# Optimization experiments

Hardware: AMD Instinct MI355X
Metric: run time of the kernel (lower is better)

## Reference

```python
import jax, jax.numpy as jnp
import numpy as np
from jax import lax

DIM = 192
HEADS = 6
WIDTH = 256
HEIGHT = 128
BATCH = 2


def _conv1x1(x, w):
    # x: [b,c,h,w], w: [o,c] (1x1 conv, no bias)
    return jnp.einsum('bchw,oc->bohw', x, w)


def setup_inputs() -> dict:
    key = jax.random.key(0)
    ks = jax.random.split(key, 7)
    c = DIM
    std = c ** -0.5
    x = jax.random.normal(ks[0], (BATCH, c, HEIGHT, WIDTH), dtype=jnp.float32)
    rpb_table = 0.02 * jax.random.normal(ks[1], (2 * WIDTH - 1, HEADS), dtype=jnp.float32)
    w_qkv = std * jax.random.normal(ks[2], (3 * c, c), dtype=jnp.float32)
    w_depth = (1.0 / 3.0) * jax.random.normal(ks[3], (3 * c, 1, 3, 3), dtype=jnp.float32)
    w_pre = std * jax.random.normal(ks[4], (c, c), dtype=jnp.float32)
    w_out = std * jax.random.normal(ks[5], (c, c), dtype=jnp.float32)
    w_gate = std * jax.random.normal(ks[6], (c, c), dtype=jnp.float32)
    return {"x": x, "rpb_table": rpb_table, "w_qkv": w_qkv, "w_depth": w_depth,
            "w_pre": w_pre, "w_out": w_out, "w_gate": w_gate, "num_heads": HEADS}


def reference(x, rpb_table, w_qkv, w_depth, w_pre, w_out, w_gate, num_heads):
    b, c, h, w = x.shape
    hd = c // num_heads
    scale = hd ** -0.5

    x_gate = jax.nn.silu(_conv1x1(x, w_gate))

    t = _conv1x1(x, w_qkv)  # [b, 3c, h, w]
    qkv = lax.conv_general_dilated(
        t, w_depth, window_strides=(1, 1), padding='SAME',
        feature_group_count=3 * c,
        dimension_numbers=('NCHW', 'OIHW', 'NCHW'))
    q, k, v = jnp.split(qkv, 3, axis=1)

    def _rows(z):
        # 'b (head c) h w -> b h head w c'
        return z.reshape(b, num_heads, hd, h, w).transpose(0, 3, 1, 4, 2)

    q = _rows(q) * scale
    k = _rows(k)
    v = _rows(v)

    attn = jnp.einsum('bhnic,bhnjc->bhnij', q, k)  # [b, h, heads, w, w]

    # relative position bias: index[i, j] = i - j + (w - 1)
    idx = jnp.arange(w)[:, None] - jnp.arange(w)[None, :] + (w - 1)
    bias = rpb_table[idx].transpose(2, 0, 1)  # [heads, w, w]
    attn = jax.nn.softmax(attn + bias[None, None], axis=-1)

    out = jnp.einsum('bhnij,bhnjc->bhnic', attn, v)
    # 'b h head w c -> b (head c) h w'
    out = out.transpose(0, 2, 4, 1, 3).reshape(b, c, h, w)

    out = _conv1x1(out, w_pre) * x_gate
    return _conv1x1(out, w_out)
```

## Files before the change

### kernel.cpp

```cpp
#include <hip/hip_runtime.h>
#include <hip/hip_bf16.h>
#include <math.h>

#define BATCH 2
#define C 192
#define H 128
#define W 256
#define HEADS 6
#define HD 32
#define HW (H * W)
#define C3 (3 * C)
#define NPX (BATCH * HW)

typedef unsigned short ushort_t;
using bf16x8 = __attribute__((ext_vector_type(8))) short;
using f32x4  = __attribute__((ext_vector_type(4))) float;

static __device__ __forceinline__ float bfbits2f(ushort_t u) {
    return __uint_as_float(((unsigned)u) << 16);
}
static __device__ __forceinline__ ushort_t f2bfbits(float f) {
    __hip_bfloat16 h = __float2bfloat16(f);
    return *reinterpret_cast<ushort_t*>(&h);
}

__global__ __launch_bounds__(256) void prep_w_kernel(
    const float* __restrict__ wq, const float* __restrict__ wg,
    const float* __restrict__ wp, const float* __restrict__ wo,
    ushort_t* __restrict__ dst)
{
    const int i = blockIdx.x * 256 + threadIdx.x;
    const float* src; int off, base;
    if (i < 27648)      { src = wq; off = i;         base = 0; }
    else if (i < 36864) { src = wg; off = i - 27648; base = 110592; }
    else if (i < 46080) { src = wp; off = i - 36864; base = 147456; }
    else                { src = wo; off = i - 46080; base = 184320; }
    float4 v = ((const float4*)src)[off];
    if (i < 9216) {
        const float sc = 0.17677669529663687f;
        v.x *= sc; v.y *= sc; v.z *= sc; v.w *= sc;
    }
    ushort4 o;
    o.x = f2bfbits(v.x); o.y = f2bfbits(v.y);
    o.z = f2bfbits(v.z); o.w = f2bfbits(v.w);
    *(ushort4*)(dst + base + off * 4) = o;
}

__global__ __launch_bounds__(256) void transpose_x_kernel(
    const float* __restrict__ x, ushort_t* __restrict__ xt)
{
    __shared__ uint Xs[64 * 97];
    const int p0 = blockIdx.x * 64;
    const int b  = p0 >> 15, hw0 = p0 & (HW - 1);
    const int t  = threadIdx.x;

    {
        const int px = t & 63, g = t >> 6;
        const float* xb = x + (size_t)b * C * HW + hw0 + px;
#pragma unroll
        for (int i = 0; i < 24; ++i) {
            const int cp = g + i * 4;
            const float v0 = xb[(size_t)(2 * cp) * HW];
            const float v1 = xb[(size_t)(2 * cp + 1) * HW];
            Xs[px * 97 + cp] = (uint)f2bfbits(v0) | ((uint)f2bfbits(v1) << 16);
        }
    }
    __syncthreads();
    {
        const int px = t >> 2, grp = t & 3;
        uint* dst = (uint*)(xt + (size_t)(p0 + px) * C) + grp * 24;
        const uint* s = &Xs[px * 97 + grp * 24];
#pragma unroll
        for (int i = 0; i < 6; ++i) {
            uint4 u;
            u.x = s[i * 4 + 0]; u.y = s[i * 4 + 1];
            u.z = s[i * 4 + 2]; u.w = s[i * 4 + 3];
            *(uint4*)(dst + i * 4) = u;
        }
    }
}

template <int MODE, int OUTKIND, int MT>
__global__ __launch_bounds__(256) void conv_mfma_kernel(
    const ushort_t* __restrict__ in_t, const ushort_t* __restrict__ w_bf,
    void* __restrict__ outp, const ushort_t* __restrict__ gate, int ostride)
{
    const int lin = blockIdx.x;
    const int xcd = lin & 7;
    const int jj  = lin >> 3;
    const int pin = jj / MT;
    const int m   = jj - pin * MT;
    const int m0  = m * 64;
    const int p0  = (xcd * 16 + pin) * 512;

    const int t  = threadIdx.x;
    const int wv = t >> 6, lane = t & 63, quad = lane >> 4, l16 = lane & 15;

    __shared__ ushort_t As[64 * 200];
    {
        const int row = t >> 2, cg = (t & 3) * 48;
        const ushort_t* src = w_bf + (size_t)(m0 + row) * C + cg;
        ushort_t* dst = &As[row * 200 + cg];
#pragma unroll
        for (int i = 0; i < 6; ++i)
            *(bf16x8*)(dst + i * 8) = *(const bf16x8*)(src + i * 8);
    }
    __syncthreads();

    f32x4 acc[4][8];
#pragma unroll
    for (int rt = 0; rt < 4; ++rt)
#pragma unroll
        for (int ct = 0; ct < 8; ++ct) acc[rt][ct] = f32x4{0.f, 0.f, 0.f, 0.f};

    const ushort_t* bp = in_t + (size_t)(p0 + wv * 128 + l16) * C + quad * 8;

    bf16x8 bF[8], bFn[8];
#pragma unroll
    for (int ct = 0; ct < 8; ++ct)
        bF[ct] = *(const bf16x8*)(bp + (size_t)(ct * 16) * C);

#pragma unroll
    for (int ks = 0; ks < 6; ++ks) {
        if (ks < 5) {
#pragma unroll
            for (int ct = 0; ct < 8; ++ct)
                bFn[ct] = *(const bf16x8*)(bp + (size_t)(ct * 16) * C +
                                           (ks + 1) * 32);
        }
        bf16x8 aF[4];
#pragma unroll
        for (int rt = 0; rt < 4; ++rt)
            aF[rt] = *(const bf16x8*)&As[(rt * 16 + l16) * 200 + quad * 8 + ks * 32];
#pragma unroll
        for (int rt = 0; rt < 4; ++rt)
#pragma unroll
            for (int ct = 0; ct < 8; ++ct)
                acc[rt][ct] = __builtin_amdgcn_mfma_f32_16x16x32_bf16(
                    aF[rt], bF[ct], acc[rt][ct], 0, 0, 0);
#pragma unroll
        for (int ct = 0; ct < 8; ++ct) bF[ct] = bFn[ct];
    }

#pragma unroll
    for (int rt = 0; rt < 4; ++rt)
#pragma unroll
        for (int ct = 0; ct < 8; ++ct) {
            f32x4 v = acc[rt][ct];
            if (MODE == 1) {
#pragma unroll
                for (int r = 0; r < 4; ++r)
                    v[r] = v[r] / (1.f + __expf(-v[r]));
            }
            acc[rt][ct] = v;
        }

    if constexpr (OUTKIND == 0) {
        ushort_t* ob = (ushort_t*)outp;
#pragma unroll
        for (int rt = 0; rt < 4; ++rt)
#pragma unroll
            for (int ct = 0; ct < 8; ++ct) {
                const int px = p0 + wv * 128 + ct * 16 + l16;
                const int ch = m0 + rt * 16 + quad * 4;
                f32x4 v = acc[rt][ct];
                if (MODE == 2) {
                    const ushort4 g = *(const ushort4*)(gate + (size_t)px * C + ch);
                    v[0] *= bfbits2f(g.x); v[1] *= bfbits2f(g.y);
                    v[2] *= bfbits2f(g.z); v[3] *= bfbits2f(g.w);
                }
                ushort4 o;
                o.x = f2bfbits(v[0]); o.y = f2bfbits(v[1]);
                o.z = f2bfbits(v[2]); o.w = f2bfbits(v[3]);
                *(ushort4*)(ob + (size_t)px * ostride + ch) = o;
            }
    } else {
        const int bb = p0 >> 15;
        const int hwb = (p0 & (HW - 1)) + wv * 128;
        float* ob = (float*)outp + ((size_t)bb * C + m0) * HW + hwb;
#pragma unroll
        for (int rt = 0; rt < 4; ++rt)
#pragma unroll
            for (int ct = 0; ct < 8; ++ct) {
                const f32x4 v = acc[rt][ct];
#pragma unroll
                for (int r = 0; r < 4; ++r)
                    ob[(size_t)(rt * 16 + quad * 4 + r) * HW + ct * 16 + l16] = v[r];
            }
    }
}

__global__ __launch_bounds__(256) void dwconv3x3_px_kernel(
    const ushort_t* __restrict__ tin, const float* __restrict__ wd,
    ushort_t* __restrict__ out)
{
    __shared__ float wloc[576];
    const int cb  = blockIdx.y;
    const int tid = threadIdx.x;
    if (tid < 144)
        *(float4*)&wloc[tid * 4] = *(const float4*)(wd + cb * 576 + tid * 4);
    __syncthreads();

    const int chloc = (tid & 7) * 8;
    const int px = blockIdx.x * 128 + (tid >> 3) * 4;
    const int x0 = px & (W - 1);
    const int y  = (px >> 8) & (H - 1);

    const ushort_t* tb = tin + (size_t)px * C3 + cb * 64 + chloc;

    float acc[4][8];
#pragma unroll
    for (int i = 0; i < 4; ++i)
#pragma unroll
        for (int k = 0; k < 8; ++k) acc[i][k] = 0.f;

#pragma unroll
    for (int dy = -1; dy <= 1; ++dy) {
        const int yy = y + dy;
        if (yy < 0 || yy >= H) continue;
        const ushort_t* rp = tb + (ptrdiff_t)dy * W * C3;

        float f[6][8];
#pragma unroll
        for (int d = 0; d < 6; ++d) {
            const int xx = x0 + d - 1;
            if (xx < 0 || xx >= W) {
#pragma unroll
                for (int k = 0; k < 8; ++k) f[d][k] = 0.f;
            } else {
                const bf16x8 v = *(const bf16x8*)(rp + (ptrdiff_t)(d - 1) * C3);
#pragma unroll
                for (int k = 0; k < 8; ++k) f[d][k] = bfbits2f((ushort_t)v[k]);
            }
        }
#pragma unroll
        for (int k = 0; k < 8; ++k) {
            const float* wk = &wloc[(chloc + k) * 9 + (dy + 1) * 3];
            const float w0 = wk[0], w1 = wk[1], w2 = wk[2];
#pragma unroll
            for (int i = 0; i < 4; ++i)
                acc[i][k] += f[i][k] * w0 + f[i + 1][k] * w1 + f[i + 2][k] * w2;
        }
    }

    ushort_t* ob = out + (size_t)px * C3 + cb * 64 + chloc;
#pragma unroll
    for (int i = 0; i < 4; ++i) {
        bf16x8 o;
#pragma unroll
        for (int k = 0; k < 8; ++k) o[k] = (short)f2bfbits(acc[i][k]);
        *(bf16x8*)(ob + (size_t)i * C3) = o;
    }
}

__global__ __launch_bounds__(256) void attention_mfma_kernel(
    const ushort_t* __restrict__ qkv, const float* __restrict__ rpb,
    ushort_t* __restrict__ att)
{
    const int y    = blockIdx.x;
    const int head = blockIdx.y;
    const int b    = blockIdx.z;
    const int t    = threadIdx.x;
    const int wv   = t >> 6;
    const int lane = t & 63;
    const int quad = lane >> 4;
    const int l16  = lane & 15;

    __shared__ __align__(16) char smem[61952];
    ushort_t* Ks  = (ushort_t*)smem;
    ushort_t* Vt  = (ushort_t*)(smem + 20480);
    ushort_t* Qs  = (ushort_t*)(smem + 37376);
    ushort_t* rb4 = (ushort_t*)(smem + 57856);
    float*    Ol  = (float*)smem;

    const ushort_t* rowp = qkv + ((size_t)b * HW + (size_t)y * W + t) * C3 +
                           head * HD;
    bf16x8 vfr[4];
#pragma unroll
    for (int g = 0; g < 4; ++g) {
        *(bf16x8*)&Qs[t * 40 + g * 8] = *(const bf16x8*)(rowp + g * 8);
        *(bf16x8*)&Ks[t * 40 + g * 8] = *(const bf16x8*)(rowp + C + g * 8);
        vfr[g] = *(const bf16x8*)(rowp + 2 * C + g * 8);
    }
#pragma unroll
    for (int g = 0; g < 4; ++g)
#pragma unroll
        for (int k = 0; k < 8; ++k)
            Vt[(g * 8 + k) * 264 + t] = (ushort_t)vfr[g][k];

#pragma unroll
    for (int s = 0; s < 4; ++s) {
        const int k1 = t, k2 = 256 + t;
        const float v1 = (k1 + s < 511) ? rpb[(k1 + s) * HEADS + head] : 0.f;
        const float v2 = (k2 + s < 511) ? rpb[(k2 + s) * HEADS + head] : 0.f;
        rb4[s * 512 + k1] = f2bfbits(v1);
        rb4[s * 512 + k2] = f2bfbits(v2);
    }
    __syncthreads();

    bf16x8 aQ[4];
#pragma unroll
    for (int rt = 0; rt < 4; ++rt) {
        const int row = wv * 64 + rt * 16 + l16;
        aQ[rt] = *(const bf16x8*)&Qs[row * 40 + quad * 8];
    }
    __syncthreads();
    ushort_t* Pb = Qs + wv * 2560;

    float l_acc[16];
#pragma unroll
    for (int i = 0; i < 16; ++i) l_acc[i] = 0.f;
    f32x4 o_acc[4][2];
#pragma unroll
    for (int rt = 0; rt < 4; ++rt)
#pragma unroll
        for (int ct = 0; ct < 2; ++ct)
            o_acc[rt][ct] = f32x4{0.f, 0.f, 0.f, 0.f};

    for (int c2 = 0; c2 < 8; ++c2) {
#pragma unroll
        for (int half = 0; half < 2; ++half) {
            const int n = c2 * 2 + half;
            const bf16x8 bK = *(const bf16x8*)&Ks[(n * 16 + l16) * 40 + quad * 8];
#pragma unroll
            for (int rt = 0; rt < 4; ++rt) {
                const int base = wv * 64 + rt * 16 + quad * 4 - (n * 16 + l16) + 255;
                const int r0 = base & 3;
                const uint2 raw = *(const uint2*)(rb4 + r0 * 512 + (base - r0));
                f32x4 s;
                s[0] = __uint_as_float(raw.x << 16);
                s[1] = __uint_as_float(raw.x & 0xffff0000u);
                s[2] = __uint_as_float(raw.y << 16);
                s[3] = __uint_as_float(raw.y & 0xffff0000u);
                s = __builtin_amdgcn_mfma_f32_16x16x32_bf16(aQ[rt], bK, s, 0, 0, 0);
#pragma unroll
                for (int reg = 0; reg < 4; ++reg) {
                    const float p = __expf(s[reg]);
                    l_acc[rt * 4 + reg] += p;
                    Pb[(rt * 16 + quad * 4 + reg) * 40 + half * 16 + l16] =
                        f2bfbits(p);
                }
            }
        }
#pragma unroll
        for (int rt = 0; rt < 4; ++rt) {
            const bf16x8 aP = *(const bf16x8*)&Pb[(rt * 16 + l16) * 40 + quad * 8];
#pragma unroll
            for (int ct = 0; ct < 2; ++ct) {
                const bf16x8 bV = *(const bf16x8*)
                    &Vt[(ct * 16 + l16) * 264 + c2 * 32 + quad * 8];
                o_acc[rt][ct] = __builtin_amdgcn_mfma_f32_16x16x32_bf16(
                    aP, bV, o_acc[rt][ct], 0, 0, 0);
            }
        }
    }

#pragma unroll
    for (int i = 0; i < 16; ++i) {
        float v = l_acc[i];
        v += __shfl_xor(v, 1);
        v += __shfl_xor(v, 2);
        v += __shfl_xor(v, 4);
        v += __shfl_xor(v, 8);
        l_acc[i] = 1.f / v;
    }

    __syncthreads();
#pragma unroll
    for (int rt = 0; rt < 4; ++rt) {
        const int i = wv * 64 + rt * 16 + quad * 4;
#pragma unroll
        for (int ct = 0; ct < 2; ++ct) {
            const int c = ct * 16 + l16;
#pragma unroll
            for (int reg = 0; reg < 4; ++reg)
                Ol[c * 257 + i + reg] = o_acc[rt][ct][reg] * l_acc[rt * 4 + reg];
        }
    }
    __syncthreads();

    ushort_t* op = att + ((size_t)b * HW + (size_t)y * W + t) * C + head * HD;
#pragma unroll
    for (int g8 = 0; g8 < 4; ++g8) {
        bf16x8 o;
#pragma unroll
        for (int k = 0; k < 8; ++k)
            o[k] = (short)f2bfbits(Ol[(g8 * 8 + k) * 257 + t]);
        *(bf16x8*)(op + g8 * 8) = o;
    }
}

extern "C" void kernel_launch(void* const* d_in, const int* in_sizes, int n_in,
                              void* d_out, int out_size, void* d_ws, size_t ws_size,
                              hipStream_t stream)
{
    const float* x       = (const float*)d_in[0];
    const float* rpb     = (const float*)d_in[1];
    const float* w_qkv   = (const float*)d_in[2];
    const float* w_depth = (const float*)d_in[3];
    const float* w_pre   = (const float*)d_in[4];
    const float* w_out   = (const float*)d_in[5];
    const float* w_gate  = (const float*)d_in[6];
    float* out = (float*)d_out;

    char* wsb = (char*)d_ws;
    ushort_t* wbf      = (ushort_t*)wsb;
    ushort_t* w_qkv_b  = wbf;
    ushort_t* w_gate_b = wbf + 110592;
    ushort_t* w_pre_b  = wbf + 147456;
    ushort_t* w_out_b  = wbf + 184320;
    ushort_t* gate_t   = (ushort_t*)(wsb + 524288u);
    ushort_t* buf_t    = (ushort_t*)(wsb + 25690112u);
    ushort_t* att_t    = (ushort_t*)(wsb + 25690112u);
    ushort_t* y_t      = (ushort_t*)(wsb + 50855936u);
    ushort_t* buf_qkv  = (ushort_t*)(wsb + 101187584u);
    ushort_t* x_t      = (ushort_t*)(wsb + 101187584u);

    dim3 blk(256);

    prep_w_kernel<<<dim3(216), blk, 0, stream>>>(w_qkv, w_gate, w_pre, w_out, wbf);
    transpose_x_kernel<<<dim3(NPX / 64), blk, 0, stream>>>(x, x_t);
    conv_mfma_kernel<1, 0, 3><<<dim3(384), blk, 0, stream>>>(
        x_t, w_gate_b, gate_t, nullptr, C);
    conv_mfma_kernel<0, 0, 9><<<dim3(1152), blk, 0, stream>>>(
        x_t, w_qkv_b, buf_t, nullptr, C3);
    dwconv3x3_px_kernel<<<dim3(NPX / 128, 9), blk, 0, stream>>>(
        buf_t, w_depth, buf_qkv);
    attention_mfma_kernel<<<dim3(H, HEADS, BATCH), blk, 0, stream>>>(
        buf_qkv, rpb, att_t);
    conv_mfma_kernel<2, 0, 3><<<dim3(384), blk, 0, stream>>>(
        att_t, w_pre_b, y_t, gate_t, C);
    conv_mfma_kernel<0, 1, 3><<<dim3(384), blk, 0, stream>>>(
        y_t, w_out_b, out, nullptr, C);
}
```

Baseline: 351.2 us.

## Restructure attention: compute S transposed, exp2 softmax, direct-global Q/K loads, smaller LDS

The attention kernel now computes the transposed score tile (K as the A operand, Q as B), so each lane holds four consecutive key columns of one query row. P can then be written to LDS as a single packed 64-bit store, and the row sums reduce with two shuffles instead of four per row. Scale and bias are pre-multiplied by log2(e) so the kernel can use the hardware exp2 directly. Q and K fragments are read straight from global memory, with the next K fragment prefetched, which removes the Q/K staging in LDS and one barrier. LDS use drops from about 62 KB to about 39 KB and launch bounds request 4 blocks per CU for higher occupancy, at the cost of uncoalesced strided global reads for the K fragments.

```diff
diff --git a/kernel.cpp b/kernel.cpp
--- a/kernel.cpp
+++ b/kernel.cpp
@@ -37,7 +37,7 @@
     else                { src = wo; off = i - 46080; base = 184320; }
     float4 v = ((const float4*)src)[off];
     if (i < 9216) {
-        const float sc = 0.17677669529663687f;
+        const float sc = 0.25503488f;
         v.x *= sc; v.y *= sc; v.z *= sc; v.w *= sc;
     }
     ushort4 o;
@@ -253,7 +253,7 @@
     }
 }
 
-__global__ __launch_bounds__(256) void attention_mfma_kernel(
+__global__ __launch_bounds__(256, 4) void attention_mfma_kernel(
     const ushort_t* __restrict__ qkv, const float* __restrict__ rpb,
     ushort_t* __restrict__ att)
 {
@@ -266,50 +266,51 @@
     const int quad = lane >> 4;
     const int l16  = lane & 15;
 
-    __shared__ __align__(16) char smem[61952];
-    ushort_t* Ks  = (ushort_t*)smem;
-    ushort_t* Vt  = (ushort_t*)(smem + 20480);
-    ushort_t* Qs  = (ushort_t*)(smem + 37376);
-    ushort_t* rb4 = (ushort_t*)(smem + 57856);
-    float*    Ol  = (float*)smem;
-
-    const ushort_t* rowp = qkv + ((size_t)b * HW + (size_t)y * W + t) * C3 +
-                           head * HD;
-    bf16x8 vfr[4];
-#pragma unroll
-    for (int g = 0; g < 4; ++g) {
-        *(bf16x8*)&Qs[t * 40 + g * 8] = *(const bf16x8*)(rowp + g * 8);
-        *(bf16x8*)&Ks[t * 40 + g * 8] = *(const bf16x8*)(rowp + C + g * 8);
-        vfr[g] = *(const bf16x8*)(rowp + 2 * C + g * 8);
-    }
-#pragma unroll
-    for (int g = 0; g < 4; ++g)
-#pragma unroll
-        for (int k = 0; k < 8; ++k)
-            Vt[(g * 8 + k) * 264 + t] = (ushort_t)vfr[g][k];
-
-#pragma unroll
-    for (int s = 0; s < 4; ++s) {
-        const int k1 = t, k2 = 256 + t;
-        const float v1 = (k1 + s < 511) ? rpb[(k1 + s) * HEADS + head] : 0.f;
-        const float v2 = (k2 + s < 511) ? rpb[(k2 + s) * HEADS + head] : 0.f;
-        rb4[s * 512 + k1] = f2bfbits(v1);
-        rb4[s * 512 + k2] = f2bfbits(v2);
-    }
-    __syncthreads();
+    __shared__ __align__(16) char smem[39424];
+    ushort_t* Vt = (ushort_t*)smem;
+    ushort_t* Pb = (ushort_t*)(smem + 16896);
+    ushort_t* rb = (ushort_t*)(smem + 37376);
+    float*    Ol = (float*)smem;
+
+    const size_t rowbase = ((size_t)b * HW + (size_t)y * W) * C3;
+    const ushort_t* qbase = qkv + rowbase + head * HD + quad * 8;
+    const ushort_t* kbase = qbase + C;
+
+    {
+        const ushort_t* rowp = qkv + rowbase + (size_t)t * C3 + head * HD;
+        bf16x8 vfr[4];
+#pragma unroll
+        for (int g = 0; g < 4; ++g)
+            vfr[g] = *(const bf16x8*)(rowp + 2 * C + g * 8);
+#pragma unroll
+        for (int g = 0; g < 4; ++g)
+#pragma unroll
+            for (int k = 0; k < 8; ++k)
+                Vt[(g * 8 + k) * 264 + t] = (ushort_t)vfr[g][k];
+    }
+    {
+        const float LOG2E = 1.4426950408889634f;
+#pragma unroll
+        for (int s2 = 0; s2 < 2; ++s2)
+#pragma unroll
+            for (int pp = 0; pp < 2; ++pp) {
+                const int k = pp * 256 + t;
+                const int src = k + s2;
+                rb[s2 * 512 + k] =
+                    f2bfbits(src <= 510 ? rpb[src * HEADS + head] * LOG2E : 0.f);
+            }
+    }
 
     bf16x8 aQ[4];
 #pragma unroll
-    for (int rt = 0; rt < 4; ++rt) {
-        const int row = wv * 64 + rt * 16 + l16;
-        aQ[rt] = *(const bf16x8*)&Qs[row * 40 + quad * 8];
-    }
-    __syncthreads();
-    ushort_t* Pb = Qs + wv * 2560;
-
-    float l_acc[16];
-#pragma unroll
-    for (int i = 0; i < 16; ++i) l_acc[i] = 0.f;
+    for (int rt = 0; rt < 4; ++rt)
+        aQ[rt] = *(const bf16x8*)(qbase + (size_t)(wv * 64 + rt * 16 + l16) * C3);
+    bf16x8 bK = *(const bf16x8*)(kbase + (size_t)l16 * C3);
+
+    __syncthreads();
+
+    ushort_t* PbW = Pb + wv * 2560;
+    float lsum[4] = {0.f, 0.f, 0.f, 0.f};
     f32x4 o_acc[4][2];
 #pragma unroll
     for (int rt = 0; rt < 4; ++rt)
@@ -317,34 +318,42 @@
         for (int ct = 0; ct < 2; ++ct)
             o_acc[rt][ct] = f32x4{0.f, 0.f, 0.f, 0.f};
 
+    const int ibase = wv * 64 + l16 + 255 - quad * 4;
+
     for (int c2 = 0; c2 < 8; ++c2) {
 #pragma unroll
         for (int half = 0; half < 2; ++half) {
-            const int n = c2 * 2 + half;
-            const bf16x8 bK = *(const bf16x8*)&Ks[(n * 16 + l16) * 40 + quad * 8];
+            const int n  = c2 * 2 + half;
+            const int nn = (n < 15) ? n + 1 : 15;
+            const bf16x8 bKn =
+                *(const bf16x8*)(kbase + (size_t)(nn * 16 + l16) * C3);
 #pragma unroll
             for (int rt = 0; rt < 4; ++rt) {
-                const int base = wv * 64 + rt * 16 + quad * 4 - (n * 16 + l16) + 255;
-                const int r0 = base & 3;
-                const uint2 raw = *(const uint2*)(rb4 + r0 * 512 + (base - r0));
+                const int a  = ibase + rt * 16 - n * 16 - 3;
+                const int s2 = a & 1;
+                const uint* tp = (const uint*)(rb + s2 * 512 + (a - s2));
+                const uint u0 = tp[0], u1 = tp[1];
                 f32x4 s;
-                s[0] = __uint_as_float(raw.x << 16);
-                s[1] = __uint_as_float(raw.x & 0xffff0000u);
-                s[2] = __uint_as_float(raw.y << 16);
-                s[3] = __uint_as_float(raw.y & 0xffff0000u);
-                s = __builtin_amdgcn_mfma_f32_16x16x32_bf16(aQ[rt], bK, s, 0, 0, 0);
-#pragma unroll
-                for (int reg = 0; reg < 4; ++reg) {
-                    const float p = __expf(s[reg]);
-                    l_acc[rt * 4 + reg] += p;
-                    Pb[(rt * 16 + quad * 4 + reg) * 40 + half * 16 + l16] =
-                        f2bfbits(p);
-                }
-            }
+                s[0] = __uint_as_float(u1 & 0xffff0000u);
+                s[1] = __uint_as_float(u1 << 16);
+                s[2] = __uint_as_float(u0 & 0xffff0000u);
+                s[3] = __uint_as_float(u0 << 16);
+                s = __builtin_amdgcn_mfma_f32_16x16x32_bf16(bK, aQ[rt], s, 0, 0, 0);
+                const float p0 = __builtin_amdgcn_exp2f(s[0]);
+                const float p1 = __builtin_amdgcn_exp2f(s[1]);
+                const float p2 = __builtin_amdgcn_exp2f(s[2]);
+                const float p3 = __builtin_amdgcn_exp2f(s[3]);
+                lsum[rt] += (p0 + p1) + (p2 + p3);
+                uint2 dd;
+                dd.x = (uint)f2bfbits(p0) | ((uint)f2bfbits(p1) << 16);
+                dd.y = (uint)f2bfbits(p2) | ((uint)f2bfbits(p3) << 16);
+                *(uint2*)&PbW[(rt * 16 + l16) * 40 + half * 16 + quad * 4] = dd;
+            }
+            bK = bKn;
         }
 #pragma unroll
         for (int rt = 0; rt < 4; ++rt) {
-            const bf16x8 aP = *(const bf16x8*)&Pb[(rt * 16 + l16) * 40 + quad * 8];
+            const bf16x8 aP = *(const bf16x8*)&PbW[(rt * 16 + l16) * 40 + quad * 8];
 #pragma unroll
             for (int ct = 0; ct < 2; ++ct) {
                 const bf16x8 bV = *(const bf16x8*)
@@ -355,26 +364,29 @@
         }
     }
 
-#pragma unroll
-    for (int i = 0; i < 16; ++i) {
-        float v = l_acc[i];
-        v += __shfl_xor(v, 1);
-        v += __shfl_xor(v, 2);
-        v += __shfl_xor(v, 4);
-        v += __shfl_xor(v, 8);
-        l_acc[i] = 1.f / v;
+    float linv[4];
+#pragma unroll
+    for (int rt = 0; rt < 4; ++rt) {
+        float v = lsum[rt];
+        v += __shfl_xor(v, 16);
+        v += __shfl_xor(v, 32);
+        linv[rt] = 1.f / v;
     }
 
     __syncthreads();
 #pragma unroll
     for (int rt = 0; rt < 4; ++rt) {
         const int i = wv * 64 + rt * 16 + quad * 4;
+        float sc[4];
+#pragma unroll
+        for (int reg = 0; reg < 4; ++reg)
+            sc[reg] = __shfl(linv[rt], quad * 4 + reg);
 #pragma unroll
         for (int ct = 0; ct < 2; ++ct) {
             const int c = ct * 16 + l16;
 #pragma unroll
             for (int reg = 0; reg < 4; ++reg)
-                Ol[c * 257 + i + reg] = o_acc[rt][ct][reg] * l_acc[rt * 4 + reg];
+                Ol[c * 257 + i + reg] = o_acc[rt][ct][reg] * sc[reg];
         }
     }
     __syncthreads();
```

Measured after the change: 328.2 us. -6.6%, faster.
